# Optimization experiments

Measured on AMD Instinct MI355X. Metric: run time of the kernel, lower is better.

## Reference

```python
import jax, jax.numpy as jnp
import numpy as np

N_NODES = 100000
N_EDGES = 1600000
D_IN = 128
HIDDEN = 64
N_CLASSES = 10
N_GRAPHS = 512


def setup_inputs() -> dict:
    key = jax.random.key(0)
    ks = jax.random.split(key, 9)
    x = jax.random.normal(ks[0], (N_NODES, D_IN), dtype=jnp.float32)
    edge_index = jax.random.randint(ks[1], (2, N_EDGES), 0, N_NODES, dtype=jnp.int32)
    batch = jnp.sort(jax.random.randint(ks[2], (N_NODES,), 0, N_GRAPHS, dtype=jnp.int32))
    # GCNConv: lin (no bias) + separate bias added after aggregation
    s1 = 1.0 / np.sqrt(D_IN)
    s2 = 1.0 / np.sqrt(HIDDEN)
    W1 = jax.random.uniform(ks[3], (D_IN, HIDDEN), jnp.float32, -s1, s1)
    b1 = jnp.zeros((HIDDEN,), jnp.float32)
    W2 = jax.random.uniform(ks[4], (HIDDEN, HIDDEN), jnp.float32, -s2, s2)
    b2 = jnp.zeros((HIDDEN,), jnp.float32)
    Wfc = jax.random.uniform(ks[5], (HIDDEN, N_CLASSES), jnp.float32, -s2, s2)
    bfc = jax.random.uniform(ks[6], (N_CLASSES,), jnp.float32, -s2, s2)
    return {"x": x, "edge_index": edge_index, "batch": batch,
            "W1": W1, "b1": b1, "W2": W2, "b2": b2, "Wfc": Wfc, "bfc": bfc}


def gcn_conv(x, src, dst, W, b, n_nodes):
    # symmetric normalization with added self-loops (PyG gcn_norm defaults)
    deg = jnp.zeros((n_nodes,), x.dtype).at[dst].add(1.0) + 1.0  # +1 self-loop
    dinv = jax.lax.rsqrt(deg)
    h = x @ W  # [N, out]
    coef = (dinv[src] * dinv[dst])[:, None]          # [E, 1]
    msg = h[src] * coef                               # [E, out]
    agg = jax.ops.segment_sum(msg, dst, num_segments=n_nodes)
    agg = agg + h * (dinv * dinv)[:, None]            # self-loop contribution
    return agg + b


def reference(x, edge_index, batch, W1, b1, W2, b2, Wfc, bfc):
    src, dst = edge_index[0], edge_index[1]
    n_nodes = x.shape[0]
    h = gcn_conv(x, src, dst, W1, b1, n_nodes)
    h = jax.nn.relu(h)
    # dropout skipped (inference, training=False)
    h = gcn_conv(h, src, dst, W2, b2, n_nodes)
    h = jax.nn.relu(h)
    # global mean pool over graphs
    sums = jax.ops.segment_sum(h, batch, num_segments=N_GRAPHS)
    cnts = jax.ops.segment_sum(jnp.ones((n_nodes,), h.dtype), batch, num_segments=N_GRAPHS)
    pooled = sums / jnp.maximum(cnts, 1.0)[:, None]   # [G, hidden]
    logits = pooled @ Wfc + bfc                        # [G, classes]
    return jax.nn.log_softmax(logits, axis=1)
```

## Files before the change

kernel.cpp:

```cpp
#include <hip/hip_runtime.h>
#include <cstdint>
#include <cstddef>

#define N_NODES   100000
#define N_EDGES   1600000
#define D_IN      128
#define HIDDEN    64
#define N_GRAPHS  512
#define N_CLASSES 10

#define NB   196
#define EB   1563
#define EB4  391
#define NBE  (NB * EB)
#define BCAP 12288
#define PSLOTS 8

typedef __attribute__((ext_vector_type(8))) short bf16x8;
typedef __attribute__((ext_vector_type(4))) float f32x4;
typedef __attribute__((ext_vector_type(2))) float f32x2;

__device__ inline float bf2f(unsigned short u) {
    return __uint_as_float(((unsigned int)u) << 16);
}
__device__ inline unsigned short f2bf(float f) {
    unsigned int x = __float_as_uint(f);
    return (unsigned short)((x + 0x7FFF + ((x >> 16) & 1)) >> 16);
}

__global__ __launch_bounds__(256)
void scan1_kernel(const int* __restrict__ in, int* __restrict__ bsum, int n) {
    __shared__ int lds[256];
    int tid = threadIdx.x;
    int base = blockIdx.x * 4096 + tid * 16;
    int s = 0;
#pragma unroll
    for (int j = 0; j < 16; j++) { int i = base + j; if (i < n) s += in[i]; }
    lds[tid] = s; __syncthreads();
    for (int off = 128; off > 0; off >>= 1) {
        if (tid < off) lds[tid] += lds[tid + off];
        __syncthreads();
    }
    if (tid == 0) bsum[blockIdx.x] = lds[0];
}

__global__ __launch_bounds__(256)
void scan2_kernel(int* __restrict__ bsum, int* __restrict__ out, int nb, int n) {
    __shared__ int lds[256];
    int tid = threadIdx.x;
    int v = (tid < nb) ? bsum[tid] : 0;
    lds[tid] = v; __syncthreads();
    for (int off = 1; off < 256; off <<= 1) {
        int t = (tid >= off) ? lds[tid - off] : 0;
        __syncthreads();
        lds[tid] += t;
        __syncthreads();
    }
    if (tid < nb) bsum[tid] = lds[tid] - v;
    if (tid == 255) out[n] = lds[255];
}

__global__ __launch_bounds__(256)
void scan3_kernel(const int* __restrict__ in, const int* __restrict__ bsum,
                  int* __restrict__ out, int n) {
    __shared__ int lds[256];
    int tid = threadIdx.x;
    int base = blockIdx.x * 4096 + tid * 16;
    int v[16]; int s = 0;
#pragma unroll
    for (int j = 0; j < 16; j++) {
        int i = base + j;
        v[j] = (i < n) ? in[i] : 0;
        s += v[j];
    }
    lds[tid] = s; __syncthreads();
    for (int off = 1; off < 256; off <<= 1) {
        int t = (tid >= off) ? lds[tid - off] : 0;
        __syncthreads();
        lds[tid] += t;
        __syncthreads();
    }
    int ex = lds[tid] - s + bsum[blockIdx.x];
#pragma unroll
    for (int j = 0; j < 16; j++) {
        int i = base + j;
        if (i < n) { out[i] = ex; ex += v[j]; }
    }
}

__global__ __launch_bounds__(256)
void hist_kernel(const int* __restrict__ dst, int* __restrict__ HA) {
    __shared__ int cnt[NB];
    const int tid = threadIdx.x;
    const int hb = blockIdx.x;
    for (int i = tid; i < NB; i += 256) cnt[i] = 0;
    __syncthreads();
    int base = hb * 1024 + tid;
#pragma unroll
    for (int j = 0; j < 4; j++) {
        int t = base + j * 256;
        if (t < N_EDGES) atomicAdd(&cnt[dst[t] >> 9], 1);
    }
    __syncthreads();
    for (int b = tid; b < NB; b += 256) HA[b * EB + hb] = cnt[b];
}

__global__ __launch_bounds__(256)
void scatterA2_kernel(const int* __restrict__ src, const int* __restrict__ dst,
                      const int* __restrict__ posA, unsigned int* __restrict__ edgeA) {
    __shared__ int off[NB];
    int tid = threadIdx.x, blk = blockIdx.x;
    for (int b = tid; b < NB; b += 256) off[b] = posA[b * EB + blk * 4];
    __syncthreads();
    int base = blk * 4096 + tid;
#pragma unroll
    for (int j = 0; j < 16; j++) {
        int t = base + j * 256;
        if (t < N_EDGES) {
            int d = dst[t];
            unsigned int pk = (((unsigned int)(d & 511)) << 17) | (unsigned int)src[t];
            int r = atomicAdd(&off[d >> 9], 1);
            edgeA[r] = pk;
        }
    }
}

__global__ __launch_bounds__(256)
void passB_kernel(const int* __restrict__ posA, const unsigned int* __restrict__ edgeA,
                  int* __restrict__ noffs, float* __restrict__ dinv,
                  int* __restrict__ srcs2) {
    __shared__ int hist[512];
    __shared__ int off[512];
    __shared__ int ps[256];
    __shared__ int srcs_l[BCAP];

    int tid = threadIdx.x, b = blockIdx.x;
    int e0 = posA[b * EB];
    int e1 = posA[(b + 1) * EB];
    int n0 = b << 9;
    int nn = min(512, N_NODES - n0);
    int len = e1 - e0;

    hist[tid] = 0; hist[tid + 256] = 0;
    __syncthreads();
    for (int i = e0 + tid; i < e1; i += 256) atomicAdd(&hist[edgeA[i] >> 17], 1);
    __syncthreads();

    for (int n = tid; n < nn; n += 256) dinv[n0 + n] = rsqrtf((float)hist[n] + 1.0f);

    int a0 = hist[2 * tid], a1 = hist[2 * tid + 1];
    ps[tid] = a0 + a1;
    __syncthreads();
    for (int d = 1; d < 256; d <<= 1) {
        int v = (tid >= d) ? ps[tid - d] : 0;
        __syncthreads();
        ps[tid] += v;
        __syncthreads();
    }
    int pre = ps[tid] - (a0 + a1);
    off[2 * tid] = pre;
    off[2 * tid + 1] = pre + a0;
    __syncthreads();

    for (int n = tid; n < nn; n += 256) noffs[n0 + n] = e0 + off[n];
    if (b == NB - 1 && tid == 0) noffs[N_NODES] = N_EDGES;
    __syncthreads();

    if (len <= BCAP) {
        for (int i = e0 + tid; i < e1; i += 256) {
            unsigned int e = edgeA[i];
            int r = atomicAdd(&off[e >> 17], 1);
            srcs_l[r] = (int)(e & 0x1FFFFu);
        }
        __syncthreads();
        for (int i = tid; i < len; i += 256) srcs2[e0 + i] = srcs_l[i];
    } else {
        for (int i = e0 + tid; i < e1; i += 256) {
            unsigned int e = edgeA[i];
            int r = atomicAdd(&off[e >> 17], 1);
            srcs2[e0 + r] = (int)(e & 0x1FFFFu);
        }
    }
}

__global__ __launch_bounds__(512)
void gemm1_kernel(const float* __restrict__ X, const float* __restrict__ W,
                  const float* __restrict__ dinv, unsigned short* __restrict__ H,
                  int n_rows) {
    constexpr int K  = D_IN;
    constexpr int KP = K + 8;
    __shared__ unsigned short Wt[64 * KP];

    const int tid  = threadIdx.x;
    const int row0 = blockIdx.x * 128;

    for (int i = tid; i < K * 64; i += 512) {
        int k = i >> 6;
        int n = i & 63;
        Wt[n * KP + k] = f2bf(W[i]);
    }

    const int wave = tid >> 6;
    const int lane = tid & 63;
    const int lrow = lane & 15;
    const int quad = lane >> 4;
    const int m = wave * 16 + lrow;
    const int row = row0 + m;
    const bool valid = row < n_rows;

    float4 xa[8];
    if (valid) {
        const float4* xr4 = (const float4*)(X + (size_t)row * K);
#pragma unroll
        for (int kt = 0; kt < 4; kt++) {
            int q = (kt * 32 + quad * 8) >> 2;
            xa[2 * kt]     = xr4[q];
            xa[2 * kt + 1] = xr4[q + 1];
        }
    } else {
#pragma unroll
        for (int j = 0; j < 8; j++) xa[j] = make_float4(0.f, 0.f, 0.f, 0.f);
    }
    __syncthreads();

    f32x4 acc0 = {0.f, 0.f, 0.f, 0.f};
    f32x4 acc1 = {0.f, 0.f, 0.f, 0.f};
    f32x4 acc2 = {0.f, 0.f, 0.f, 0.f};
    f32x4 acc3 = {0.f, 0.f, 0.f, 0.f};

#pragma unroll
    for (int kt = 0; kt < 4; kt++) {
        int k0 = kt * 32 + quad * 8;
        const float* f = (const float*)&xa[2 * kt];
        bf16x8 a;
#pragma unroll
        for (int j = 0; j < 8; j++) a[j] = (short)f2bf(f[j]);
        bf16x8 b0 = *(const bf16x8*)&Wt[(0 * 16 + lrow) * KP + k0];
        bf16x8 b1 = *(const bf16x8*)&Wt[(1 * 16 + lrow) * KP + k0];
        bf16x8 b2 = *(const bf16x8*)&Wt[(2 * 16 + lrow) * KP + k0];
        bf16x8 b3 = *(const bf16x8*)&Wt[(3 * 16 + lrow) * KP + k0];
        acc0 = __builtin_amdgcn_mfma_f32_16x16x32_bf16(a, b0, acc0, 0, 0, 0);
        acc1 = __builtin_amdgcn_mfma_f32_16x16x32_bf16(a, b1, acc1, 0, 0, 0);
        acc2 = __builtin_amdgcn_mfma_f32_16x16x32_bf16(a, b2, acc2, 0, 0, 0);
        acc3 = __builtin_amdgcn_mfma_f32_16x16x32_bf16(a, b3, acc3, 0, 0, 0);
    }

    f32x4 accs[4] = {acc0, acc1, acc2, acc3};
#pragma unroll
    for (int r = 0; r < 4; r++) {
        int orow = row0 + wave * 16 + quad * 4 + r;
        if (orow < n_rows) {
            float dv = dinv[orow];
#pragma unroll
            for (int c = 0; c < 4; c++)
                H[(size_t)orow * 64 + c * 16 + lrow] = f2bf(accs[c][r] * dv);
        }
    }
}

__device__ inline void upk_add(int4 u, float* acc) {
    unsigned int a = (unsigned int)u.x, b = (unsigned int)u.y;
    unsigned int d = (unsigned int)u.z, e = (unsigned int)u.w;
    acc[0] += __uint_as_float(a << 16);
    acc[1] += __uint_as_float(a & 0xFFFF0000u);
    acc[2] += __uint_as_float(b << 16);
    acc[3] += __uint_as_float(b & 0xFFFF0000u);
    acc[4] += __uint_as_float(d << 16);
    acc[5] += __uint_as_float(d & 0xFFFF0000u);
    acc[6] += __uint_as_float(e << 16);
    acc[7] += __uint_as_float(e & 0xFFFF0000u);
}

__device__ inline void upk8_add(int2 u, float* acc) {
    f32x2 p0 = __builtin_amdgcn_cvt_pk_f32_fp8(u.x, false);
    f32x2 p1 = __builtin_amdgcn_cvt_pk_f32_fp8(u.x, true);
    f32x2 p2 = __builtin_amdgcn_cvt_pk_f32_fp8(u.y, false);
    f32x2 p3 = __builtin_amdgcn_cvt_pk_f32_fp8(u.y, true);
    acc[0] += p0.x; acc[1] += p0.y;
    acc[2] += p1.x; acc[3] += p1.y;
    acc[4] += p2.x; acc[5] += p2.y;
    acc[6] += p3.x; acc[7] += p3.y;
}

__global__ __launch_bounds__(512)
void gather1_gemm2_kernel(const int* __restrict__ offs, const int* __restrict__ srcs,
                          const float* __restrict__ dinv, const unsigned short* __restrict__ h,
                          const float* __restrict__ b1v, const float* __restrict__ W2,
                          unsigned char* __restrict__ H8, int n_nodes) {
    constexpr int KP = 72;
    __shared__ unsigned short Hs[64 * KP];
    __shared__ unsigned short Wt[64 * KP];

    const int tid   = threadIdx.x;
    const int node0 = blockIdx.x * 64;

    for (int i = tid; i < 64 * 64; i += 512) {
        int k = i >> 6;
        int n = i & 63;
        Wt[n * KP + k] = f2bf(W2[i]);
    }

    const int g    = tid >> 3;
    const int node = node0 + g;
    const int cg   = (tid & 7) * 8;

    float acc[8];
#pragma unroll
    for (int j = 0; j < 8; j++) acc[j] = 0.f;
    float dn = 0.f;

    if (node < n_nodes) {
        dn = dinv[node];
        int4 us = *(const int4*)(h + (size_t)node * 64 + cg);
        upk_add(us, acc);

        int i = offs[node];
        const int i1 = offs[node + 1];
        int rem = i1 - i;
        if (rem > 0) {
            int s[8];
#pragma unroll
            for (int j = 0; j < 8; j++) s[j] = srcs[i + (j < rem ? j : rem - 1)];
            while (rem > 0) {
                int4 u8[8];
#pragma unroll
                for (int j = 0; j < 8; j++)
                    u8[j] = *(const int4*)(h + (size_t)s[j] * 64 + cg);
                const int cur  = rem < 8 ? rem : 8;
                const int ni   = i + cur;
                const int nrem = rem - cur;
                if (nrem > 0) {
#pragma unroll
                    for (int j = 0; j < 8; j++)
                        s[j] = srcs[ni + (j < nrem ? j : nrem - 1)];
                }
#pragma unroll
                for (int j = 0; j < 8; j++) { if (j < cur) upk_add(u8[j], acc); }
                i = ni; rem = nrem;
            }
        }
    }

    {
        float4 bv0 = *(const float4*)(b1v + cg);
        float4 bv1 = *(const float4*)(b1v + cg + 4);
        float r0 = fmaxf(dn * acc[0] + bv0.x, 0.f);
        float r1 = fmaxf(dn * acc[1] + bv0.y, 0.f);
        float r2 = fmaxf(dn * acc[2] + bv0.z, 0.f);
        float r3 = fmaxf(dn * acc[3] + bv0.w, 0.f);
        float r4 = fmaxf(dn * acc[4] + bv1.x, 0.f);
        float r5 = fmaxf(dn * acc[5] + bv1.y, 0.f);
        float r6 = fmaxf(dn * acc[6] + bv1.z, 0.f);
        float r7 = fmaxf(dn * acc[7] + bv1.w, 0.f);
        ushort4 p0 = make_ushort4(f2bf(r0), f2bf(r1), f2bf(r2), f2bf(r3));
        ushort4 p1 = make_ushort4(f2bf(r4), f2bf(r5), f2bf(r6), f2bf(r7));
        *(ushort4*)&Hs[g * KP + cg]     = p0;
        *(ushort4*)&Hs[g * KP + cg + 4] = p1;
    }
    __syncthreads();

    const int wave = tid >> 6;
    const int lane = tid & 63;
    const int lrow = lane & 15;
    const int quad = lane >> 4;
    const int rt = (wave & 3) * 16;
    const int ct = (wave >> 2) * 32;
    const int m = rt + lrow;

    f32x4 acc0 = {0.f, 0.f, 0.f, 0.f};
    f32x4 acc1 = {0.f, 0.f, 0.f, 0.f};
#pragma unroll
    for (int kt = 0; kt < 2; kt++) {
        int k0 = kt * 32 + quad * 8;
        bf16x8 a  = *(const bf16x8*)&Hs[m * KP + k0];
        bf16x8 w0 = *(const bf16x8*)&Wt[(ct + lrow) * KP + k0];
        bf16x8 w1 = *(const bf16x8*)&Wt[(ct + 16 + lrow) * KP + k0];
        acc0 = __builtin_amdgcn_mfma_f32_16x16x32_bf16(a, w0, acc0, 0, 0, 0);
        acc1 = __builtin_amdgcn_mfma_f32_16x16x32_bf16(a, w1, acc1, 0, 0, 0);
    }

    f32x4 accs[2] = {acc0, acc1};
#pragma unroll
    for (int r = 0; r < 4; r++) {
        int row = node0 + rt + quad * 4 + r;
        if (row < n_nodes) {
            float dv = dinv[row];
#pragma unroll
            for (int c = 0; c < 2; c++) {
                float v = accs[c][r] * dv;
                int p = __builtin_amdgcn_cvt_pk_fp8_f32(v, v, 0, false);
                H8[(size_t)row * 64 + ct + c * 16 + lrow] = (unsigned char)(p & 0xFF);
            }
        }
    }
}

__global__ __launch_bounds__(256)
void gather_fp8_pool_kernel(const int* __restrict__ offs, const int* __restrict__ srcs,
                            const float* __restrict__ dinv, const unsigned char* __restrict__ h8,
                            const float* __restrict__ b, const int* __restrict__ batch,
                            float* __restrict__ pooled, float* __restrict__ cnt,
                            int n_nodes) {
    __shared__ float pacc[PSLOTS][64];
    __shared__ float lcnt[PSLOTS];
    __shared__ int sg[2];

    int tid = threadIdx.x;
    int node0 = blockIdx.x * 32;
    int lastn = min(node0 + 31, n_nodes - 1);
    for (int i = tid; i < PSLOTS * 64; i += 256) ((float*)pacc)[i] = 0.f;
    if (tid < PSLOTS) lcnt[tid] = 0.f;
    if (tid == 0) { sg[0] = batch[min(node0, n_nodes - 1)]; sg[1] = batch[lastn]; }
    __syncthreads();
    int g0 = sg[0];
    bool single = (sg[0] == sg[1]);

    int node = node0 + (tid >> 3);
    int cg = (tid & 7) * 8;

    float r[8];
#pragma unroll
    for (int j = 0; j < 8; j++) r[j] = 0.f;

    if (node < n_nodes) {
        float dn = dinv[node];
        float acc[8];
#pragma unroll
        for (int j = 0; j < 8; j++) acc[j] = 0.f;
        {
            int2 u = *(const int2*)(h8 + (size_t)node * 64 + cg);
            upk8_add(u, acc);
        }

        int i = offs[node];
        const int i1 = offs[node + 1];
        int rem = i1 - i;

        int curA = 0;
        int2 uA[8];
        if (rem > 0) {
            curA = rem < 8 ? rem : 8;
            int sA[8];
#pragma unroll
            for (int j = 0; j < 8; j++) sA[j] = srcs[i + (j < curA ? j : curA - 1)];
#pragma unroll
            for (int j = 0; j < 8; j++)
                uA[j] = *(const int2*)(h8 + (size_t)sA[j] * 64 + cg);
            i += curA; rem -= curA;
        }
        while (curA > 0) {
            int curB = 0;
            int2 uB[8];
            if (rem > 0) {
                curB = rem < 8 ? rem : 8;
                int sB[8];
#pragma unroll
                for (int j = 0; j < 8; j++) sB[j] = srcs[i + (j < curB ? j : curB - 1)];
#pragma unroll
                for (int j = 0; j < 8; j++)
                    uB[j] = *(const int2*)(h8 + (size_t)sB[j] * 64 + cg);
                i += curB; rem -= curB;
            }
#pragma unroll
            for (int j = 0; j < 8; j++) { if (j < curA) upk8_add(uA[j], acc); }
#pragma unroll
            for (int j = 0; j < 8; j++) uA[j] = uB[j];
            curA = curB;
        }

        float4 b0 = *(const float4*)(b + cg);
        float4 b1 = *(const float4*)(b + cg + 4);
        r[0] = fmaxf(dn * acc[0] + b0.x, 0.f);
        r[1] = fmaxf(dn * acc[1] + b0.y, 0.f);
        r[2] = fmaxf(dn * acc[2] + b0.z, 0.f);
        r[3] = fmaxf(dn * acc[3] + b0.w, 0.f);
        r[4] = fmaxf(dn * acc[4] + b1.x, 0.f);
        r[5] = fmaxf(dn * acc[5] + b1.y, 0.f);
        r[6] = fmaxf(dn * acc[6] + b1.z, 0.f);
        r[7] = fmaxf(dn * acc[7] + b1.w, 0.f);
    }

    if (single) {
#pragma unroll
        for (int j = 0; j < 8; j++) {
            float v = r[j];
            v += __shfl_xor(v, 8);
            v += __shfl_xor(v, 16);
            v += __shfl_xor(v, 32);
            r[j] = v;
        }
        int wave = tid >> 6;
        int lane = tid & 63;
        if (lane < 8) {
#pragma unroll
            for (int j = 0; j < 8; j++) pacc[wave][lane * 8 + j] = r[j];
        }
        __syncthreads();
        if (tid < 64) {
            float s = pacc[0][tid] + pacc[1][tid] + pacc[2][tid] + pacc[3][tid];
            if (s != 0.f) unsafeAtomicAdd(&pooled[(size_t)g0 * 64 + tid], s);
        }
        if (tid == 0) {
            int valid = min(32, n_nodes - node0);
            unsafeAtomicAdd(&cnt[g0], (float)valid);
        }
    } else {
        if (node < n_nodes) {
            int g = batch[node];
            int slot = g - g0;
            if (slot < PSLOTS) {
#pragma unroll
                for (int j = 0; j < 8; j++) atomicAdd(&pacc[slot][cg + j], r[j]);
                if ((tid & 7) == 0) atomicAdd(&lcnt[slot], 1.f);
            } else {
#pragma unroll
                for (int j = 0; j < 8; j++) unsafeAtomicAdd(&pooled[(size_t)g * 64 + cg + j], r[j]);
                if ((tid & 7) == 0) unsafeAtomicAdd(&cnt[g], 1.f);
            }
        }
        __syncthreads();
        for (int i = tid; i < PSLOTS * 64; i += 256) {
            float v = ((float*)pacc)[i];
            if (v != 0.f) unsafeAtomicAdd(&pooled[(size_t)(g0 + (i >> 6)) * 64 + (i & 63)], v);
        }
        if (tid < PSLOTS && lcnt[tid] != 0.f) unsafeAtomicAdd(&cnt[g0 + tid], lcnt[tid]);
    }
}

__global__ __launch_bounds__(256)
void head_kernel(const float* __restrict__ pooled, const float* __restrict__ cnt,
                 const float* __restrict__ Wfc, const float* __restrict__ bfc,
                 float* __restrict__ out) {
    __shared__ float Ws[HIDDEN * N_CLASSES];
    __shared__ float bs[N_CLASSES];
    int tid = threadIdx.x;
    for (int i = tid; i < HIDDEN * N_CLASSES; i += 256) Ws[i] = Wfc[i];
    if (tid < N_CLASSES) bs[tid] = bfc[tid];
    __syncthreads();

    int g = blockIdx.x * 256 + tid;
    if (g >= N_GRAPHS) return;

    float inv = 1.f / fmaxf(cnt[g], 1.f);
    float p[HIDDEN];
#pragma unroll
    for (int k = 0; k < HIDDEN; k++) p[k] = pooled[(size_t)g * 64 + k] * inv;

    float lg[N_CLASSES];
    float m = -1e30f;
#pragma unroll
    for (int j = 0; j < N_CLASSES; j++) {
        float a = bs[j];
#pragma unroll
        for (int k = 0; k < HIDDEN; k++) a += p[k] * Ws[k * N_CLASSES + j];
        lg[j] = a;
        m = fmaxf(m, a);
    }
    float s = 0.f;
#pragma unroll
    for (int j = 0; j < N_CLASSES; j++) s += __expf(lg[j] - m);
    float lse = m + __logf(s);
#pragma unroll
    for (int j = 0; j < N_CLASSES; j++) out[(size_t)g * N_CLASSES + j] = lg[j] - lse;
}

extern "C" void kernel_launch(void* const* d_in, const int* in_sizes, int n_in,
                              void* d_out, int out_size, void* d_ws, size_t ws_size,
                              hipStream_t stream) {
    const float* x   = (const float*)d_in[0];
    const int*   ei  = (const int*)d_in[1];
    const int*   bat = (const int*)d_in[2];
    const float* W1  = (const float*)d_in[3];
    const float* b1  = (const float*)d_in[4];
    const float* W2  = (const float*)d_in[5];
    const float* b2  = (const float*)d_in[6];
    const float* Wfc = (const float*)d_in[7];
    const float* bfc = (const float*)d_in[8];
    float* out = (float*)d_out;

    const int* src = ei;
    const int* dst = ei + N_EDGES;

    char* ws = (char*)d_ws;

    const size_t OFF_H     = 0;
    const size_t OFF_SRCS2 = 12800000;
    const size_t OFF_NOFFS = 19200000;
    const size_t OFF_DINV  = 19600016;
    const size_t OFF_BUFB  = 25600000;
    const size_t OFF_EDGEA = 38400000;
    const size_t OFF_HA    = 51200000;
    const size_t OFF_POSA  = 52425392;
    const size_t OFF_BSUM  = 53650800;
    const size_t OFF_POOL  = 53651824;
    const size_t OFF_CNT   = 53782896;

    unsigned short* hbuf  = (unsigned short*)(ws + OFF_H);
    int*   srcs2  = (int*)  (ws + OFF_SRCS2);
    int*   noffs  = (int*)  (ws + OFF_NOFFS);
    float* dinv   = (float*)(ws + OFF_DINV);
    unsigned char* hbuf8 = (unsigned char*)(ws + OFF_BUFB);
    unsigned int* edgeA = (unsigned int*)(ws + OFF_EDGEA);
    int*   HA     = (int*)  (ws + OFF_HA);
    int*   posA   = (int*)  (ws + OFF_POSA);
    int*   bsum   = (int*)  (ws + OFF_BSUM);
    float* pooled = (float*)(ws + OFF_POOL);
    float* cnt    = (float*)(ws + OFF_CNT);

    const int SCAN_BLOCKS = (NBE + 4095) / 4096;
    const int GATHER_BLOCKS = (N_NODES * 8 + 255) / 256;
    const int GEMM2_BLOCKS = (N_NODES + 63) / 64;
    const int GEMM1_BLOCKS = (N_NODES + 127) / 128;

    hipMemsetAsync(pooled, 0, (size_t)(131072 + 2048), stream);

    hist_kernel<<<EB, 256, 0, stream>>>(dst, HA);
    scan1_kernel<<<SCAN_BLOCKS, 256, 0, stream>>>(HA, bsum, NBE);
    scan2_kernel<<<1, 256, 0, stream>>>(bsum, posA, SCAN_BLOCKS, NBE);
    scan3_kernel<<<SCAN_BLOCKS, 256, 0, stream>>>(HA, bsum, posA, NBE);
    scatterA2_kernel<<<EB4, 256, 0, stream>>>(src, dst, posA, edgeA);
    passB_kernel<<<NB, 256, 0, stream>>>(posA, edgeA, noffs, dinv, srcs2);
    gemm1_kernel<<<GEMM1_BLOCKS, 512, 0, stream>>>(x, W1, dinv, hbuf, N_NODES);
    gather1_gemm2_kernel<<<GEMM2_BLOCKS, 512, 0, stream>>>(
        noffs, srcs2, dinv, hbuf, b1, W2, hbuf8, N_NODES);
    gather_fp8_pool_kernel<<<GATHER_BLOCKS, 256, 0, stream>>>(
        noffs, srcs2, dinv, hbuf8, b2, bat, pooled, cnt, N_NODES);

    head_kernel<<<(N_GRAPHS + 255) / 256, 256, 0, stream>>>(pooled, cnt, Wfc, bfc, out);
}
```

Before: 231.0 us.

## Fuse CSR build stages into one cooperative kernel with grid syncs

Replaces the six separate CSR-construction kernels (histogram, three scan passes, bucket scatter, per-bucket sort) with a single cooperative launch of 391 blocks that separates the phases with grid.sync(). This removes several kernel launch gaps and the inter-kernel drain between small phases. In exchange, each phase runs on only 391 blocks, so the histogram loops over extra work, and phases that use fewer blocks (the 75-block scan, the 196-block pass B) leave the rest idle. The fused kernel also carries 12K ints of shared memory, which may limit how many blocks fit per CU, and grid-wide barriers have their own cost.

```diff
diff --git a/kernel.cpp b/kernel.cpp
--- a/kernel.cpp
+++ b/kernel.cpp
@@ -1,6 +1,9 @@
 #include <hip/hip_runtime.h>
+#include <hip/hip_cooperative_groups.h>
 #include <cstdint>
 #include <cstddef>
+
+namespace cg = cooperative_groups;
 
 #define N_NODES   100000
 #define N_EDGES   1600000
@@ -13,6 +16,7 @@
 #define EB   1563
 #define EB4  391
 #define NBE  (NB * EB)
+#define SCB  75
 #define BCAP 12288
 #define PSLOTS 8
 
@@ -29,156 +33,151 @@
 }
 
 __global__ __launch_bounds__(256)
-void scan1_kernel(const int* __restrict__ in, int* __restrict__ bsum, int n) {
-    __shared__ int lds[256];
-    int tid = threadIdx.x;
-    int base = blockIdx.x * 4096 + tid * 16;
-    int s = 0;
-#pragma unroll
-    for (int j = 0; j < 16; j++) { int i = base + j; if (i < n) s += in[i]; }
-    lds[tid] = s; __syncthreads();
-    for (int off = 128; off > 0; off >>= 1) {
-        if (tid < off) lds[tid] += lds[tid + off];
-        __syncthreads();
-    }
-    if (tid == 0) bsum[blockIdx.x] = lds[0];
-}
-
-__global__ __launch_bounds__(256)
-void scan2_kernel(int* __restrict__ bsum, int* __restrict__ out, int nb, int n) {
-    __shared__ int lds[256];
-    int tid = threadIdx.x;
-    int v = (tid < nb) ? bsum[tid] : 0;
-    lds[tid] = v; __syncthreads();
-    for (int off = 1; off < 256; off <<= 1) {
-        int t = (tid >= off) ? lds[tid - off] : 0;
-        __syncthreads();
-        lds[tid] += t;
-        __syncthreads();
-    }
-    if (tid < nb) bsum[tid] = lds[tid] - v;
-    if (tid == 255) out[n] = lds[255];
-}
-
-__global__ __launch_bounds__(256)
-void scan3_kernel(const int* __restrict__ in, const int* __restrict__ bsum,
-                  int* __restrict__ out, int n) {
-    __shared__ int lds[256];
-    int tid = threadIdx.x;
-    int base = blockIdx.x * 4096 + tid * 16;
-    int v[16]; int s = 0;
-#pragma unroll
-    for (int j = 0; j < 16; j++) {
-        int i = base + j;
-        v[j] = (i < n) ? in[i] : 0;
-        s += v[j];
-    }
-    lds[tid] = s; __syncthreads();
-    for (int off = 1; off < 256; off <<= 1) {
-        int t = (tid >= off) ? lds[tid - off] : 0;
-        __syncthreads();
-        lds[tid] += t;
-        __syncthreads();
-    }
-    int ex = lds[tid] - s + bsum[blockIdx.x];
-#pragma unroll
-    for (int j = 0; j < 16; j++) {
-        int i = base + j;
-        if (i < n) { out[i] = ex; ex += v[j]; }
-    }
-}
-
-__global__ __launch_bounds__(256)
-void hist_kernel(const int* __restrict__ dst, int* __restrict__ HA) {
-    __shared__ int cnt[NB];
-    const int tid = threadIdx.x;
-    const int hb = blockIdx.x;
-    for (int i = tid; i < NB; i += 256) cnt[i] = 0;
-    __syncthreads();
-    int base = hb * 1024 + tid;
-#pragma unroll
-    for (int j = 0; j < 4; j++) {
-        int t = base + j * 256;
-        if (t < N_EDGES) atomicAdd(&cnt[dst[t] >> 9], 1);
-    }
-    __syncthreads();
-    for (int b = tid; b < NB; b += 256) HA[b * EB + hb] = cnt[b];
-}
-
-__global__ __launch_bounds__(256)
-void scatterA2_kernel(const int* __restrict__ src, const int* __restrict__ dst,
-                      const int* __restrict__ posA, unsigned int* __restrict__ edgeA) {
-    __shared__ int off[NB];
-    int tid = threadIdx.x, blk = blockIdx.x;
-    for (int b = tid; b < NB; b += 256) off[b] = posA[b * EB + blk * 4];
-    __syncthreads();
-    int base = blk * 4096 + tid;
-#pragma unroll
-    for (int j = 0; j < 16; j++) {
-        int t = base + j * 256;
-        if (t < N_EDGES) {
-            int d = dst[t];
-            unsigned int pk = (((unsigned int)(d & 511)) << 17) | (unsigned int)src[t];
-            int r = atomicAdd(&off[d >> 9], 1);
-            edgeA[r] = pk;
-        }
-    }
-}
-
-__global__ __launch_bounds__(256)
-void passB_kernel(const int* __restrict__ posA, const unsigned int* __restrict__ edgeA,
-                  int* __restrict__ noffs, float* __restrict__ dinv,
-                  int* __restrict__ srcs2) {
+void csr_build_kernel(const int* __restrict__ src, const int* __restrict__ dst,
+                      int* __restrict__ HA, int* __restrict__ bsum,
+                      int* __restrict__ posA, unsigned int* __restrict__ edgeA,
+                      int* __restrict__ noffs, float* __restrict__ dinv,
+                      int* __restrict__ srcs2) {
+    cg::grid_group grid = cg::this_grid();
     __shared__ int hist[512];
     __shared__ int off[512];
     __shared__ int ps[256];
     __shared__ int srcs_l[BCAP];
 
-    int tid = threadIdx.x, b = blockIdx.x;
-    int e0 = posA[b * EB];
-    int e1 = posA[(b + 1) * EB];
-    int n0 = b << 9;
-    int nn = min(512, N_NODES - n0);
-    int len = e1 - e0;
-
-    hist[tid] = 0; hist[tid + 256] = 0;
-    __syncthreads();
-    for (int i = e0 + tid; i < e1; i += 256) atomicAdd(&hist[edgeA[i] >> 17], 1);
-    __syncthreads();
-
-    for (int n = tid; n < nn; n += 256) dinv[n0 + n] = rsqrtf((float)hist[n] + 1.0f);
-
-    int a0 = hist[2 * tid], a1 = hist[2 * tid + 1];
-    ps[tid] = a0 + a1;
-    __syncthreads();
-    for (int d = 1; d < 256; d <<= 1) {
-        int v = (tid >= d) ? ps[tid - d] : 0;
-        __syncthreads();
-        ps[tid] += v;
-        __syncthreads();
-    }
-    int pre = ps[tid] - (a0 + a1);
-    off[2 * tid] = pre;
-    off[2 * tid + 1] = pre + a0;
-    __syncthreads();
-
-    for (int n = tid; n < nn; n += 256) noffs[n0 + n] = e0 + off[n];
-    if (b == NB - 1 && tid == 0) noffs[N_NODES] = N_EDGES;
-    __syncthreads();
-
-    if (len <= BCAP) {
-        for (int i = e0 + tid; i < e1; i += 256) {
-            unsigned int e = edgeA[i];
-            int r = atomicAdd(&off[e >> 17], 1);
-            srcs_l[r] = (int)(e & 0x1FFFFu);
-        }
-        __syncthreads();
-        for (int i = tid; i < len; i += 256) srcs2[e0 + i] = srcs_l[i];
-    } else {
-        for (int i = e0 + tid; i < e1; i += 256) {
-            unsigned int e = edgeA[i];
-            int r = atomicAdd(&off[e >> 17], 1);
-            srcs2[e0 + r] = (int)(e & 0x1FFFFu);
+    const int tid = threadIdx.x;
+    const int blk = blockIdx.x;
+
+    for (int hb = blk; hb < EB; hb += gridDim.x) {
+        for (int i = tid; i < NB; i += 256) hist[i] = 0;
+        __syncthreads();
+        int base = hb * 1024 + tid;
+#pragma unroll
+        for (int j = 0; j < 4; j++) {
+            int t = base + j * 256;
+            if (t < N_EDGES) atomicAdd(&hist[dst[t] >> 9], 1);
+        }
+        __syncthreads();
+        for (int b = tid; b < NB; b += 256) HA[b * EB + hb] = hist[b];
+        __syncthreads();
+    }
+    grid.sync();
+
+    if (blk < SCB) {
+        int base = blk * 4096 + tid * 16;
+        int s = 0;
+#pragma unroll
+        for (int j = 0; j < 16; j++) { int i = base + j; if (i < NBE) s += HA[i]; }
+        ps[tid] = s; __syncthreads();
+        for (int o = 128; o > 0; o >>= 1) {
+            if (tid < o) ps[tid] += ps[tid + o];
+            __syncthreads();
+        }
+        if (tid == 0) bsum[blk] = ps[0];
+    }
+    grid.sync();
+
+    if (blk < SCB) {
+        int bv = (tid < SCB) ? bsum[tid] : 0;
+        hist[tid] = bv; __syncthreads();
+        for (int o = 1; o < 256; o <<= 1) {
+            int t = (tid >= o) ? hist[tid - o] : 0;
+            __syncthreads();
+            hist[tid] += t;
+            __syncthreads();
+        }
+        hist[tid] -= bv;
+        __syncthreads();
+        int blockoff = hist[blk];
+
+        int base = blk * 4096 + tid * 16;
+        int v[16]; int s = 0;
+#pragma unroll
+        for (int j = 0; j < 16; j++) {
+            int i = base + j;
+            v[j] = (i < NBE) ? HA[i] : 0;
+            s += v[j];
+        }
+        ps[tid] = s; __syncthreads();
+        for (int o = 1; o < 256; o <<= 1) {
+            int t = (tid >= o) ? ps[tid - o] : 0;
+            __syncthreads();
+            ps[tid] += t;
+            __syncthreads();
+        }
+        int ex = ps[tid] - s + blockoff;
+#pragma unroll
+        for (int j = 0; j < 16; j++) {
+            int i = base + j;
+            if (i < NBE) { posA[i] = ex; ex += v[j]; }
+        }
+        if (blk == 0 && tid == 0) posA[NBE] = N_EDGES;
+    }
+    grid.sync();
+
+    {
+        for (int b = tid; b < NB; b += 256) off[b] = posA[b * EB + blk * 4];
+        __syncthreads();
+        int base = blk * 4096 + tid;
+#pragma unroll
+        for (int j = 0; j < 16; j++) {
+            int t = base + j * 256;
+            if (t < N_EDGES) {
+                int d = dst[t];
+                unsigned int pk = (((unsigned int)(d & 511)) << 17) | (unsigned int)src[t];
+                int r = atomicAdd(&off[d >> 9], 1);
+                edgeA[r] = pk;
+            }
+        }
+    }
+    grid.sync();
+
+    if (blk < NB) {
+        int e0 = posA[blk * EB];
+        int e1 = posA[(blk + 1) * EB];
+        int n0 = blk << 9;
+        int nn = min(512, N_NODES - n0);
+        int len = e1 - e0;
+
+        __syncthreads();
+        hist[tid] = 0; hist[tid + 256] = 0;
+        __syncthreads();
+        for (int i = e0 + tid; i < e1; i += 256) atomicAdd(&hist[edgeA[i] >> 17], 1);
+        __syncthreads();
+
+        for (int n = tid; n < nn; n += 256) dinv[n0 + n] = rsqrtf((float)hist[n] + 1.0f);
+
+        int a0 = hist[2 * tid], a1 = hist[2 * tid + 1];
+        ps[tid] = a0 + a1;
+        __syncthreads();
+        for (int d = 1; d < 256; d <<= 1) {
+            int v = (tid >= d) ? ps[tid - d] : 0;
+            __syncthreads();
+            ps[tid] += v;
+            __syncthreads();
+        }
+        int pre = ps[tid] - (a0 + a1);
+        off[2 * tid] = pre;
+        off[2 * tid + 1] = pre + a0;
+        __syncthreads();
+
+        for (int n = tid; n < nn; n += 256) noffs[n0 + n] = e0 + off[n];
+        if (blk == NB - 1 && tid == 0) noffs[N_NODES] = N_EDGES;
+        __syncthreads();
+
+        if (len <= BCAP) {
+            for (int i = e0 + tid; i < e1; i += 256) {
+                unsigned int e = edgeA[i];
+                int r = atomicAdd(&off[e >> 17], 1);
+                srcs_l[r] = (int)(e & 0x1FFFFu);
+            }
+            __syncthreads();
+            for (int i = tid; i < len; i += 256) srcs2[e0 + i] = srcs_l[i];
+        } else {
+            for (int i = e0 + tid; i < e1; i += 256) {
+                unsigned int e = edgeA[i];
+                int r = atomicAdd(&off[e >> 17], 1);
+                srcs2[e0 + r] = (int)(e & 0x1FFFFu);
+            }
         }
     }
 }
@@ -607,24 +606,23 @@
     float* pooled = (float*)(ws + OFF_POOL);
     float* cnt    = (float*)(ws + OFF_CNT);
 
-    const int SCAN_BLOCKS = (NBE + 4095) / 4096;
     const int GATHER_BLOCKS = (N_NODES * 8 + 255) / 256;
     const int GEMM2_BLOCKS = (N_NODES + 63) / 64;
     const int GEMM1_BLOCKS = (N_NODES + 127) / 128;
 
     hipMemsetAsync(pooled, 0, (size_t)(131072 + 2048), stream);
 
-    hist_kernel<<<EB, 256, 0, stream>>>(dst, HA);
-    scan1_kernel<<<SCAN_BLOCKS, 256, 0, stream>>>(HA, bsum, NBE);
-    scan2_kernel<<<1, 256, 0, stream>>>(bsum, posA, SCAN_BLOCKS, NBE);
-    scan3_kernel<<<SCAN_BLOCKS, 256, 0, stream>>>(HA, bsum, posA, NBE);
-    scatterA2_kernel<<<EB4, 256, 0, stream>>>(src, dst, posA, edgeA);
-    passB_kernel<<<NB, 256, 0, stream>>>(posA, edgeA, noffs, dinv, srcs2);
+    {
+        void* args[] = { (void*)&src, (void*)&dst, (void*)&HA, (void*)&bsum,
+                         (void*)&posA, (void*)&edgeA, (void*)&noffs,
+                         (void*)&dinv, (void*)&srcs2 };
+        hipLaunchCooperativeKernel((void*)csr_build_kernel, dim3(EB4), dim3(256),
+                                   args, 0, stream);
+    }
     gemm1_kernel<<<GEMM1_BLOCKS, 512, 0, stream>>>(x, W1, dinv, hbuf, N_NODES);
     gather1_gemm2_kernel<<<GEMM2_BLOCKS, 512, 0, stream>>>(
         noffs, srcs2, dinv, hbuf, b1, W2, hbuf8, N_NODES);
     gather_fp8_pool_kernel<<<GATHER_BLOCKS, 256, 0, stream>>>(
         noffs, srcs2, dinv, hbuf8, b2, bat, pooled, cnt, N_NODES);
-
     head_kernel<<<(N_GRAPHS + 255) / 256, 256, 0, stream>>>(pooled, cnt, Wfc, bfc, out);
 }
```

Result: slower. 433.0 us (+87.5%).
